# Kernel tuning notes

Measured on AMD Instinct MI355X. Metric: run time of the kernel, lower is better.

Reference implementation:

```python
import jax, jax.numpy as jnp
import numpy as np

B, S, H = 4, 4096, 256
WINDOW = 128


def setup_inputs() -> dict:
    key = jax.random.key(0)
    ks = jax.random.split(key, 7)
    s = 1.0 / np.sqrt(H)
    return {
        "x": jax.random.normal(ks[0], (B, S, H), dtype=jnp.float32),
        "Wq": jax.random.normal(ks[1], (H, H), dtype=jnp.float32) * s,
        "bq": jax.random.normal(ks[2], (H,), dtype=jnp.float32) * s,
        "Wk": jax.random.normal(ks[3], (H, H), dtype=jnp.float32) * s,
        "bk": jax.random.normal(ks[4], (H,), dtype=jnp.float32) * s,
        "Wv": jax.random.normal(ks[5], (H, H), dtype=jnp.float32) * s,
        "bv": jax.random.normal(ks[6], (H,), dtype=jnp.float32) * s,
        "window_size": WINDOW,
    }


def reference(x, Wq, bq, Wk, bk, Wv, bv, window_size):
    # x: [B, S, H]
    seq_len = x.shape[1]
    hidden = x.shape[2]
    scale = jnp.sqrt(jnp.asarray(hidden, dtype=x.dtype))
    q = jnp.einsum('bsh,hd->bsd', x, Wq) + bq
    k = jnp.einsum('bsh,hd->bsd', x, Wk) + bk
    v = jnp.einsum('bsh,hd->bsd', x, Wv) + bv
    scores = jnp.einsum('bsd,btd->bst', q, k) / scale  # [B, S, S]
    idx = jnp.arange(seq_len)
    band = jnp.abs(idx[:, None] - idx[None, :]) <= window_size  # [S, S]
    neg_inf = jnp.asarray(-jnp.inf, dtype=scores.dtype)
    scores = jnp.where(band[None, :, :], scores, neg_inf)
    weights = jax.nn.softmax(scores, axis=-1)
    context = jnp.einsum('bst,btd->bsd', weights, v)  # [B, S, H]
    return context.mean(axis=1)  # [B, H]
```

## Files before the change

### kernel.cpp

```cpp
#include <hip/hip_runtime.h>

#define SDIM 4096
#define HDIM 256
#define WIN 128
#define NROW 16384
#define QSCALE 0.0625f

typedef __attribute__((ext_vector_type(8))) short bf16x8;
typedef __attribute__((ext_vector_type(4))) float f32x4;

static __device__ __forceinline__ unsigned short f2bf(float f) {
  unsigned int u = __float_as_uint(f);
  return (unsigned short)((u + 0x7fffu + ((u >> 16) & 1u)) >> 16);
}

#define MFMA16(a, b, c) __builtin_amdgcn_mfma_f32_16x16x32_bf16((a), (b), (c), 0, 0, 0)


__global__ __launch_bounds__(256) void wconv(const float* __restrict__ Wq,
                                             const float* __restrict__ Wk,
                                             const float* __restrict__ Wv,
                                             unsigned short* __restrict__ Wp) {
  const int m = blockIdx.y, nt = blockIdx.x;
  const float* __restrict__ W = (m == 0) ? Wq : (m == 1) ? Wk : Wv;
  const int tid = threadIdx.x, lane = tid & 63, w = tid >> 6;
  const int l15 = lane & 15, g = lane >> 4;
#pragma unroll
  for (int half = 0; half < 2; ++half) {
    int kk = w * 2 + half;
    bf16x8 v;
#pragma unroll
    for (int j = 0; j < 8; ++j)
      v[j] = (short)f2bf(W[(size_t)(32 * kk + 8 * g + j) * HDIM + 16 * nt + l15]);
    *(bf16x8*)(Wp + ((size_t)(m * 16 + nt) * 8 + kk) * 512 + (size_t)lane * 8) = v;
  }
}

__global__ __launch_bounds__(256) void qkv_mfma(
    const float* __restrict__ x, const unsigned short* __restrict__ Wp,
    const float* __restrict__ bq, const float* __restrict__ bk,
    const float* __restrict__ bv, unsigned short* __restrict__ Qp,
    unsigned short* __restrict__ Kp, unsigned short* __restrict__ Vp) {
  __shared__ unsigned short st[32][264];
  const int tid = threadIdx.x;
  const int lane = tid & 63, w = tid >> 6;
  const int l15 = lane & 15, g = lane >> 4;
  const size_t rb = (size_t)blockIdx.x * 32;
#pragma unroll
  for (int it = 0; it < 8; ++it) {
    int u = it * 256 + tid;
    int r = u >> 6, c4 = (u & 63) << 2;
    float4 f = *(const float4*)(x + (rb + r) * HDIM + c4);
    st[r][c4 + 0] = f2bf(f.x);
    st[r][c4 + 1] = f2bf(f.y);
    st[r][c4 + 2] = f2bf(f.z);
    st[r][c4 + 3] = f2bf(f.w);
  }
  __syncthreads();
  bf16x8 a[2][8];
#pragma unroll
  for (int rtl = 0; rtl < 2; ++rtl)
#pragma unroll
    for (int kk = 0; kk < 8; ++kk)
      a[rtl][kk] = *(const bf16x8*)&st[16 * rtl + l15][32 * kk + 8 * g];
  __syncthreads();
  const int tg0 = blockIdx.x * 2;
  for (int m = 0; m < 3; ++m) {
    const unsigned short* Wm = Wp + (size_t)m * 65536;
    const float* bias = (m == 0) ? bq : (m == 1) ? bk : bv;
#pragma unroll
    for (int ntl = 0; ntl < 4; ++ntl) {
      const int nt = 4 * w + ntl;
      const unsigned short* wp_ = Wm + (size_t)nt * 4096 + (size_t)lane * 8;
      bf16x8 wf[8];
#pragma unroll
      for (int kk = 0; kk < 8; ++kk) wf[kk] = *(const bf16x8*)(wp_ + kk * 512);
      f32x4 a0 = {0.f, 0.f, 0.f, 0.f}, a1 = {0.f, 0.f, 0.f, 0.f};
#pragma unroll
      for (int kk = 0; kk < 8; ++kk) {
        a0 = MFMA16(a[0][kk], wf[kk], a0);
        a1 = MFMA16(a[1][kk], wf[kk], a1);
      }
      float bn = bias[nt * 16 + l15];
#pragma unroll
      for (int r = 0; r < 4; ++r) {
        st[4 * g + r][nt * 16 + l15] = f2bf(a0[r] + bn);
        st[16 + 4 * g + r][nt * 16 + l15] = f2bf(a1[r] + bn);
      }
    }
    __syncthreads();
    if (m < 2) {
      unsigned short* O = (m == 0 ? Qp : Kp);
#pragma unroll
      for (int it = 0; it < 4; ++it) {
        int u = it * 256 + tid;
        int ln = u & 63, kk = (u >> 6) & 7, tgl = u >> 9;
        int lg = ln >> 4, lc = ln & 15;
        bf16x8 vv = *(const bf16x8*)&st[16 * tgl + lc][32 * kk + 8 * lg];
        *(bf16x8*)(O + ((size_t)(tg0 + tgl) * 8 + kk) * 512 + (size_t)ln * 8) = vv;
      }
    } else {
#pragma unroll
      for (int it = 0; it < 4; ++it) {
        int u = it * 256 + tid;
        int lc = u & 15, gg = (u >> 4) & 1, dt = (u >> 5) & 15, tgl = u >> 9;
        bf16x8 vv;
#pragma unroll
        for (int j = 0; j < 8; ++j)
          vv[j] = (short)st[16 * tgl + 8 * gg + j][16 * dt + lc];
        *(bf16x8*)(Vp + (size_t)(tg0 + tgl) * 4096 +
                   (size_t)(dt * 32 + gg * 16 + lc) * 8) = vv;
      }
    }
    __syncthreads();
  }
}

__global__ __launch_bounds__(256) void attn_mfma(
    const unsigned short* __restrict__ Qp, const unsigned short* __restrict__ Kp,
    const unsigned short* __restrict__ Vp, float* __restrict__ partial) {
  __shared__ unsigned short plds[4][2][16][40];
  __shared__ float lsh[4][16];
  __shared__ float linv[16];
  __shared__ float fbuf[4][256];
  const int tid = threadIdx.x;
  const int lane = tid & 63, w = tid >> 6;
  const int bid = blockIdx.x;
  const int blk = (bid & 7) * 128 + (bid >> 3);
  const int b = blk >> 8;
  const int qt = blk & 255;
  const int s0 = qt << 4;
  const int l15 = lane & 15, g = lane >> 4;
  bf16x8 qf[8];
  const unsigned short* qp_ = Qp + ((size_t)b * 256 + qt) * 4096 + (size_t)lane * 8;
#pragma unroll
  for (int kk = 0; kk < 8; ++kk) qf[kk] = *(const bf16x8*)(qp_ + kk * 512);
  const unsigned short* Kb = Kp + (size_t)b * 1048576;
  const unsigned short* Vb = Vp + (size_t)b * 1048576;
  f32x4 acc[16];
  const f32x4 zero = {0.f, 0.f, 0.f, 0.f};
#pragma unroll
  for (int i = 0; i < 16; ++i) acc[i] = zero;
  float lacc[4] = {0.f, 0.f, 0.f, 0.f};
  const int cb = 2 * w;
  const int ce = (w == 3) ? 9 : 2 * w + 2;
  for (int c = cb; c < ce; ++c) {
    const int t0 = s0 - WIN + c * 32;
    if (t0 + 32 <= 0 || t0 >= SDIM) continue;
    const int tg = t0 >> 4;
    const int tga = min(max(tg, 0), 255);
    const unsigned short* kap = Kb + (size_t)tga * 4096 + (size_t)lane * 8;
    f32x4 sA = zero, sB = zero;
    const bool full = (c != 8);
    if (full) {
      const int tgb = min(max(tg + 1, 0), 255);
      const unsigned short* kbp = Kb + (size_t)tgb * 4096 + (size_t)lane * 8;
#pragma unroll
      for (int kk = 0; kk < 8; ++kk) {
        sA = MFMA16(qf[kk], *(const bf16x8*)(kap + kk * 512), sA);
        sB = MFMA16(qf[kk], *(const bf16x8*)(kbp + kk * 512), sB);
      }
    } else {
#pragma unroll
      for (int kk = 0; kk < 8; ++kk)
        sA = MFMA16(qf[kk], *(const bf16x8*)(kap + kk * 512), sA);
    }
    float p0[4], p1[4];
#pragma unroll
    for (int r = 0; r < 4; ++r) {
      int s = s0 + 4 * g + r;
      int ta = t0 + l15, tb = t0 + 16 + l15;
      bool okA = (ta >= 0) && (ta < SDIM) && (ta - s <= WIN) && (ta - s >= -WIN);
      bool okB = full && (tb >= 0) && (tb < SDIM) && (tb - s <= WIN) && (tb - s >= -WIN);
      p0[r] = okA ? __expf(sA[r] * QSCALE) : 0.f;
      p1[r] = okB ? __expf(sB[r] * QSCALE) : 0.f;
    }
#pragma unroll
    for (int r = 0; r < 4; ++r) {
      float v = p0[r] + p1[r];
      v += __shfl_xor(v, 1);
      v += __shfl_xor(v, 2);
      v += __shfl_xor(v, 4);
      v += __shfl_xor(v, 8);
      lacc[r] += v;
    }
    const int bsel = c & 1;
#pragma unroll
    for (int r = 0; r < 4; ++r) {
      plds[w][bsel][4 * g + r][l15] = f2bf(p0[r]);
      plds[w][bsel][4 * g + r][16 + l15] = f2bf(p1[r]);
    }
    bf16x8 pa = *(const bf16x8*)&plds[w][bsel][l15][8 * g];
    const int tgv = min(max(tg + (g >> 1), 0), 255);
    const unsigned short* vp_ =
        Vb + (size_t)tgv * 4096 + (size_t)(g & 1) * 128 + (size_t)l15 * 8;
#pragma unroll
    for (int dt = 0; dt < 16; ++dt)
      acc[dt] = MFMA16(pa, *(const bf16x8*)(vp_ + dt * 256), acc[dt]);
  }
  if (l15 == 0) {
#pragma unroll
    for (int r = 0; r < 4; ++r) lsh[w][4 * g + r] = lacc[r];
  }
  __syncthreads();
  if (tid < 16)
    linv[tid] = 1.0f / (lsh[0][tid] + lsh[1][tid] + lsh[2][tid] + lsh[3][tid]);
  __syncthreads();
  float li[4];
#pragma unroll
  for (int r = 0; r < 4; ++r) li[r] = linv[4 * g + r];
#pragma unroll
  for (int dt = 0; dt < 16; ++dt) {
    float s = acc[dt][0] * li[0] + acc[dt][1] * li[1] + acc[dt][2] * li[2] +
              acc[dt][3] * li[3];
    s += __shfl_xor(s, 16);
    s += __shfl_xor(s, 32);
    if (lane < 16) fbuf[w][dt * 16 + lane] = s;
  }
  __syncthreads();
  partial[(size_t)blk * HDIM + tid] =
      fbuf[0][tid] + fbuf[1][tid] + fbuf[2][tid] + fbuf[3][tid];
}

__global__ __launch_bounds__(256) void reduce_partials(
    const float* __restrict__ partial, float* __restrict__ out) {
  __shared__ float red[16][17];
  const int cx = blockIdx.x, b = blockIdx.y;
  const int lc = threadIdx.x & 15, rg = threadIdx.x >> 4;
  float s = 0.f;
#pragma unroll
  for (int i = 0; i < 16; ++i)
    s += partial[((size_t)b * 256 + rg * 16 + i) * HDIM + cx * 16 + lc];
  red[rg][lc] = s;
  __syncthreads();
  if (rg == 0) {
    float t = 0.f;
#pragma unroll
    for (int r = 0; r < 16; ++r) t += red[r][lc];
    out[(size_t)b * HDIM + cx * 16 + lc] = t * (1.0f / (float)SDIM);
  }
}

extern "C" void kernel_launch(void* const* d_in, const int* in_sizes, int n_in,
                              void* d_out, int out_size, void* d_ws, size_t ws_size,
                              hipStream_t stream) {
  const float* x  = (const float*)d_in[0];
  const float* Wq = (const float*)d_in[1];
  const float* bq = (const float*)d_in[2];
  const float* Wk = (const float*)d_in[3];
  const float* bk = (const float*)d_in[4];
  const float* Wv = (const float*)d_in[5];
  const float* bv = (const float*)d_in[6];
  float* out = (float*)d_out;

  unsigned short* Wp = (unsigned short*)d_ws;
  unsigned short* Qp = Wp + 3 * 65536;
  unsigned short* Kp = Qp + (size_t)NROW * HDIM;
  unsigned short* Vp = Kp + (size_t)NROW * HDIM;
  float* partial = (float*)(Vp + (size_t)NROW * HDIM);

  dim3 wg(16, 3);
  wconv<<<wg, 256, 0, stream>>>(Wq, Wk, Wv, Wp);
  qkv_mfma<<<512, 256, 0, stream>>>(x, Wp, bq, bk, bv, Qp, Kp, Vp);
  attn_mfma<<<1024, 256, 0, stream>>>(Qp, Kp, Vp, partial);
  dim3 rg(16, 4);
  reduce_partials<<<rg, 256, 0, stream>>>(partial, out);
}
```

Before: 51.76 us.

## Fuse weight conversion into QKV kernel with flag sync and 64-row tiles

```diff
diff --git a/kernel.cpp b/kernel.cpp
--- a/kernel.cpp
+++ b/kernel.cpp
@@ -5,6 +5,7 @@
 #define WIN 128
 #define NROW 16384
 #define QSCALE 0.0625f
+#define MAGIC 0x7F3A9C51u
 
 typedef __attribute__((ext_vector_type(8))) short bf16x8;
 typedef __attribute__((ext_vector_type(4))) float f32x4;
@@ -17,37 +18,45 @@
 #define MFMA16(a, b, c) __builtin_amdgcn_mfma_f32_16x16x32_bf16((a), (b), (c), 0, 0, 0)
 
 
-__global__ __launch_bounds__(256) void wconv(const float* __restrict__ Wq,
-                                             const float* __restrict__ Wk,
-                                             const float* __restrict__ Wv,
-                                             unsigned short* __restrict__ Wp) {
-  const int m = blockIdx.y, nt = blockIdx.x;
-  const float* __restrict__ W = (m == 0) ? Wq : (m == 1) ? Wk : Wv;
-  const int tid = threadIdx.x, lane = tid & 63, w = tid >> 6;
-  const int l15 = lane & 15, g = lane >> 4;
-#pragma unroll
-  for (int half = 0; half < 2; ++half) {
-    int kk = w * 2 + half;
-    bf16x8 v;
-#pragma unroll
-    for (int j = 0; j < 8; ++j)
-      v[j] = (short)f2bf(W[(size_t)(32 * kk + 8 * g + j) * HDIM + 16 * nt + l15]);
-    *(bf16x8*)(Wp + ((size_t)(m * 16 + nt) * 8 + kk) * 512 + (size_t)lane * 8) = v;
-  }
-}
-
 __global__ __launch_bounds__(256) void qkv_mfma(
-    const float* __restrict__ x, const unsigned short* __restrict__ Wp,
-    const float* __restrict__ bq, const float* __restrict__ bk,
-    const float* __restrict__ bv, unsigned short* __restrict__ Qp,
-    unsigned short* __restrict__ Kp, unsigned short* __restrict__ Vp) {
-  __shared__ unsigned short st[32][264];
+    const float* __restrict__ x,
+    const float* __restrict__ Wq, const float* __restrict__ Wk,
+    const float* __restrict__ Wv, const float* __restrict__ bq,
+    const float* __restrict__ bk, const float* __restrict__ bv,
+    unsigned short* __restrict__ Wp, unsigned short* __restrict__ Qp,
+    unsigned short* __restrict__ Kp, unsigned short* __restrict__ Vp,
+    unsigned* __restrict__ sent) {
+  __shared__ unsigned short st[64][264];
   const int tid = threadIdx.x;
   const int lane = tid & 63, w = tid >> 6;
   const int l15 = lane & 15, g = lane >> 4;
-  const size_t rb = (size_t)blockIdx.x * 32;
-#pragma unroll
-  for (int it = 0; it < 8; ++it) {
+  const int blk = blockIdx.x;
+
+  if (blk < 48) {
+    const int m = blk >> 4, nt = blk & 15;
+    const float* __restrict__ W = (m == 0) ? Wq : (m == 1) ? Wk : Wv;
+#pragma unroll
+    for (int it = 0; it < 2; ++it) {
+      int u = it * 256 + tid;
+      int kk = u >> 6, ln = u & 63;
+      int lg = ln >> 4, lc = ln & 15;
+      bf16x8 v;
+#pragma unroll
+      for (int j = 0; j < 8; ++j)
+        v[j] = (short)f2bf(W[(size_t)(32 * kk + 8 * lg + j) * HDIM + 16 * nt + lc]);
+      *(bf16x8*)(Wp + ((size_t)(m * 16 + nt) * 8 + kk) * 512 + (size_t)ln * 8) = v;
+    }
+    __syncthreads();
+    if (tid == 0) {
+      __threadfence();
+      __hip_atomic_store(sent + blk, MAGIC, __ATOMIC_RELEASE,
+                         __HIP_MEMORY_SCOPE_AGENT);
+    }
+  }
+
+  const size_t rb = (size_t)blk * 64;
+#pragma unroll
+  for (int it = 0; it < 16; ++it) {
     int u = it * 256 + tid;
     int r = u >> 6, c4 = (u & 63) << 2;
     float4 f = *(const float4*)(x + (rb + r) * HDIM + c4);
@@ -57,42 +66,53 @@
     st[r][c4 + 3] = f2bf(f.w);
   }
   __syncthreads();
-  bf16x8 a[2][8];
-#pragma unroll
-  for (int rtl = 0; rtl < 2; ++rtl)
+  bf16x8 a[4][8];
+#pragma unroll
+  for (int rt = 0; rt < 4; ++rt)
 #pragma unroll
     for (int kk = 0; kk < 8; ++kk)
-      a[rtl][kk] = *(const bf16x8*)&st[16 * rtl + l15][32 * kk + 8 * g];
-  __syncthreads();
-  const int tg0 = blockIdx.x * 2;
+      a[rt][kk] = *(const bf16x8*)&st[16 * rt + l15][32 * kk + 8 * g];
+  __syncthreads();
+
+  if (tid < 48) {
+    while (__hip_atomic_load(sent + tid, __ATOMIC_ACQUIRE,
+                             __HIP_MEMORY_SCOPE_AGENT) != MAGIC)
+      __builtin_amdgcn_s_sleep(2);
+  }
+  __syncthreads();
+
+  const int tg0 = blk * 4;
+  const int nt0 = 4 * w;
   for (int m = 0; m < 3; ++m) {
     const unsigned short* Wm = Wp + (size_t)m * 65536;
     const float* bias = (m == 0) ? bq : (m == 1) ? bk : bv;
 #pragma unroll
     for (int ntl = 0; ntl < 4; ++ntl) {
-      const int nt = 4 * w + ntl;
+      const int nt = nt0 + ntl;
       const unsigned short* wp_ = Wm + (size_t)nt * 4096 + (size_t)lane * 8;
       bf16x8 wf[8];
 #pragma unroll
       for (int kk = 0; kk < 8; ++kk) wf[kk] = *(const bf16x8*)(wp_ + kk * 512);
-      f32x4 a0 = {0.f, 0.f, 0.f, 0.f}, a1 = {0.f, 0.f, 0.f, 0.f};
+      f32x4 ac[4];
+#pragma unroll
+      for (int rt = 0; rt < 4; ++rt) ac[rt] = (f32x4){0.f, 0.f, 0.f, 0.f};
 #pragma unroll
       for (int kk = 0; kk < 8; ++kk) {
-        a0 = MFMA16(a[0][kk], wf[kk], a0);
-        a1 = MFMA16(a[1][kk], wf[kk], a1);
+#pragma unroll
+        for (int rt = 0; rt < 4; ++rt) ac[rt] = MFMA16(a[rt][kk], wf[kk], ac[rt]);
       }
       float bn = bias[nt * 16 + l15];
 #pragma unroll
-      for (int r = 0; r < 4; ++r) {
-        st[4 * g + r][nt * 16 + l15] = f2bf(a0[r] + bn);
-        st[16 + 4 * g + r][nt * 16 + l15] = f2bf(a1[r] + bn);
-      }
+      for (int rt = 0; rt < 4; ++rt)
+#pragma unroll
+        for (int r = 0; r < 4; ++r)
+          st[16 * rt + 4 * g + r][nt * 16 + l15] = f2bf(ac[rt][r] + bn);
     }
     __syncthreads();
     if (m < 2) {
       unsigned short* O = (m == 0 ? Qp : Kp);
 #pragma unroll
-      for (int it = 0; it < 4; ++it) {
+      for (int it = 0; it < 8; ++it) {
         int u = it * 256 + tid;
         int ln = u & 63, kk = (u >> 6) & 7, tgl = u >> 9;
         int lg = ln >> 4, lc = ln & 15;
@@ -101,7 +121,7 @@
       }
     } else {
 #pragma unroll
-      for (int it = 0; it < 4; ++it) {
+      for (int it = 0; it < 8; ++it) {
         int u = it * 256 + tid;
         int lc = u & 15, gg = (u >> 4) & 1, dt = (u >> 5) & 15, tgl = u >> 9;
         bf16x8 vv;
@@ -258,10 +278,10 @@
   unsigned short* Kp = Qp + (size_t)NROW * HDIM;
   unsigned short* Vp = Kp + (size_t)NROW * HDIM;
   float* partial = (float*)(Vp + (size_t)NROW * HDIM);
-
-  dim3 wg(16, 3);
-  wconv<<<wg, 256, 0, stream>>>(Wq, Wk, Wv, Wp);
-  qkv_mfma<<<512, 256, 0, stream>>>(x, Wp, bq, bk, bv, Qp, Kp, Vp);
+  unsigned* sent = (unsigned*)(partial + (size_t)1024 * HDIM);
+
+  qkv_mfma<<<256, 256, 0, stream>>>(x, Wq, Wk, Wv, bq, bk, bv, Wp, Qp, Kp, Vp,
+                                    sent);
   attn_mfma<<<1024, 256, 0, stream>>>(Qp, Kp, Vp, partial);
   dim3 rg(16, 4);
   reduce_partials<<<rg, 256, 0, stream>>>(partial, out);
```

After: 52.63 us. About the same (+1.7%).
